# Performance work log

Hardware: AMD Instinct MI355X
Metric: run time of the kernel (lower is better)

## Reference

```python
import jax, jax.numpy as jnp
import numpy as np

B, T, D, F = 4, 2048, 4096, 16384
EQN = 'btd,df->btf'  # fixed einsum equation (contracting axis = D, axis 0 of kernel)


def setup_inputs() -> dict:
    key = jax.random.key(0)
    k1, k2, k3 = jax.random.split(key, 3)
    x = jax.random.normal(k1, (B, T, D), dtype=jnp.float32)
    # int8-quantized kernel weights stored as integers
    kernel = jax.random.randint(k2, (D, F), -127, 128, dtype=jnp.int32).astype(jnp.int8)
    # per-output-channel dequant scale, shape (1, F) per deduce_scale_shape
    scale = jax.random.uniform(k3, (1, F), dtype=jnp.float32, minval=0.5, maxval=1.5)
    return {"x": x, "kernel": kernel, "scale": scale}


def reference(x, kernel, scale):
    # dequantize: cast int kernel to activation dtype, divide by per-channel scale
    k = kernel.astype(x.dtype) / scale  # [D, F]
    return jnp.einsum(EQN, x, k)  # [B, T, F]
```

## Files before the change

kernel.cpp:

```cpp
#include <hip/hip_runtime.h>


namespace {

constexpr int MD = 8192;
constexpr int ND = 16384;
constexpr int KD = 4096;
constexpr int NT = KD / 64;

typedef float fl4 __attribute__((ext_vector_type(4)));
typedef unsigned int u32x4 __attribute__((ext_vector_type(4)));
typedef int i32x4 __attribute__((ext_vector_type(4)));

__device__ __forceinline__ unsigned int pack4(fl4 v, float sc) {
  int q0 = __float2int_rn(v.x * sc);
  int q1 = __float2int_rn(v.y * sc);
  int q2 = __float2int_rn(v.z * sc);
  int q3 = __float2int_rn(v.w * sc);
  return (q0 & 0xFF) | ((q1 & 0xFF) << 8) | ((q2 & 0xFF) << 16) |
         ((q3 & 0xFF) << 24);
}

__global__ __launch_bounds__(256) void quant_x_kernel(
    const float* __restrict__ x, signed char* __restrict__ xq,
    float* __restrict__ xs) {
  const int row = blockIdx.x;
  const int t   = threadIdx.x;
  const float* xr = x + (size_t)row * KD + t * 16;
  fl4 v0 = *(const fl4*)(xr);
  fl4 v1 = *(const fl4*)(xr + 4);
  fl4 v2 = *(const fl4*)(xr + 8);
  fl4 v3 = *(const fl4*)(xr + 12);
  float m = 0.f;
  m = fmaxf(m, fmaxf(fmaxf(fabsf(v0.x), fabsf(v0.y)), fmaxf(fabsf(v0.z), fabsf(v0.w))));
  m = fmaxf(m, fmaxf(fmaxf(fabsf(v1.x), fabsf(v1.y)), fmaxf(fabsf(v1.z), fabsf(v1.w))));
  m = fmaxf(m, fmaxf(fmaxf(fabsf(v2.x), fabsf(v2.y)), fmaxf(fabsf(v2.z), fabsf(v2.w))));
  m = fmaxf(m, fmaxf(fmaxf(fabsf(v3.x), fabsf(v3.y)), fmaxf(fabsf(v3.z), fabsf(v3.w))));
#pragma unroll
  for (int off = 32; off; off >>= 1) m = fmaxf(m, __shfl_xor(m, off));
  __shared__ float red[4];
  if ((t & 63) == 0) red[t >> 6] = m;
  __syncthreads();
  m = fmaxf(fmaxf(red[0], red[1]), fmaxf(red[2], red[3]));
  const float sc = (m > 0.f) ? 127.0f / m : 0.f;
  if (t == 0) xs[row] = (m > 0.f) ? m / 127.0f : 0.f;
  u32x4 o;
  o.x = pack4(v0, sc);
  o.y = pack4(v1, sc);
  o.z = pack4(v2, sc);
  o.w = pack4(v3, sc);
  *(u32x4*)(xq + (size_t)row * KD + t * 16) = o;
}

__global__ __launch_bounds__(256) void transpose_w_kernel(
    const int* __restrict__ W, signed char* __restrict__ WT) {
  constexpr int KC = 64;
  const int nb = blockIdx.x & 63;
  const int kb = blockIdx.x >> 6;
  const int n  = nb * 256 + threadIdx.x;
  const int k0 = kb * KC;
  const int* src = W + (size_t)k0 * ND + n;
  unsigned int buf[16];
#pragma unroll
  for (int i = 0; i < KC; i += 4) {
    unsigned int b0 = (unsigned)src[(size_t)(i + 0) * ND] & 0xFF;
    unsigned int b1 = (unsigned)src[(size_t)(i + 1) * ND] & 0xFF;
    unsigned int b2 = (unsigned)src[(size_t)(i + 2) * ND] & 0xFF;
    unsigned int b3 = (unsigned)src[(size_t)(i + 3) * ND] & 0xFF;
    buf[i >> 2] = b0 | (b1 << 8) | (b2 << 16) | (b3 << 24);
  }
  u32x4* dst = (u32x4*)(WT + (size_t)n * KD + k0);
#pragma unroll
  for (int j = 0; j < 4; ++j) {
    u32x4 o;
    o.x = buf[4 * j + 0];
    o.y = buf[4 * j + 1];
    o.z = buf[4 * j + 2];
    o.w = buf[4 * j + 3];
    dst[j] = o;
  }
}


#define GLL16(g, l)                                                  \
  __builtin_amdgcn_global_load_lds(                                  \
      (const __attribute__((address_space(1))) void*)(g),            \
      (__attribute__((address_space(3))) void*)(l), 16, 0, 0)

#define BARRIER()    __builtin_amdgcn_s_barrier()
#define WAITL(N)     asm volatile("s_waitcnt lgkmcnt(" #N ")")
#define WAITV(N)     asm volatile("s_waitcnt vmcnt(" #N ")")
#define SCHED()      __builtin_amdgcn_sched_barrier(0)
#define PRIO1()      __builtin_amdgcn_s_setprio(1)
#define PRIO0()      __builtin_amdgcn_s_setprio(0)

__device__ __forceinline__ void stage_op(const signed char* g0, char* lbase,
                                         int w) {
  GLL16(g0, lbase + w * 1024);
  GLL16(g0 + (size_t)128 * KD, lbase + 8192 + w * 1024);
}

__global__ __launch_bounds__(512, 2) void gemm_kernel(
    const signed char* __restrict__ Aq8,
    const signed char* __restrict__ Bq8,
    const float* __restrict__ xs,
    const float* __restrict__ scale,
    float* __restrict__ C) {
  __shared__ __align__(16) char Asm[2][16384];
  __shared__ __align__(16) char Bsm[2][16384];

  const int tid  = threadIdx.x;
  const int lane = tid & 63;
  const int w    = tid >> 6;
  const int wm   = w >> 2;
  const int wn   = w & 3;

  const int bid = blockIdx.x;
  const int xcd = bid & 7;
  const int pos = bid >> 3;
  const int tm  = (xcd << 2) | (pos & 3);
  const int tn  = pos >> 2;
  const size_t brow = (size_t)tm * 256;
  const size_t bcol = (size_t)tn * 256;

  const int srow  = w * 16 + (lane >> 2);
  const int sgran = (lane & 3) ^ ((lane >> 3) & 3);
  const signed char* Ag = Aq8 + (brow + srow) * (size_t)KD + sgran * 16;
  const signed char* Bg = Bq8 + (bcol + srow) * (size_t)KD + sgran * 16;

  const int r15  = lane & 15;
  const int kcsw = (((lane >> 4) ^ ((r15 >> 1) & 3)) << 4);

  i32x4 acc[8][4];
#pragma unroll
  for (int i = 0; i < 8; ++i)
#pragma unroll
    for (int j = 0; j < 4; ++j) acc[i][j] = (i32x4){0, 0, 0, 0};

  stage_op(Ag,      &Asm[0][0], w);
  stage_op(Bg,      &Bsm[0][0], w);
  stage_op(Ag + 64, &Asm[1][0], w);
  stage_op(Bg + 64, &Bsm[1][0], w);
  SCHED();
  WAITV(4);
  SCHED();
  BARRIER();
  SCHED();

  i32x4 a[8], b[4];
  {
    const char* A0 = &Asm[0][0] + wm * 8192;
#pragma unroll
    for (int mi = 0; mi < 4; ++mi)
      a[mi] = *(const i32x4*)(A0 + (mi * 16 + r15) * 64 + kcsw);
  }
  SCHED();

#pragma unroll 2
  for (int it = 0; it < NT; ++it) {
    const int h = it & 1;
    const char* Ard  = &Asm[h][0] + wm * 8192;
    const char* ArdN = &Asm[h ^ 1][0] + wm * 8192;
    const char* Brd  = &Bsm[h][0] + wn * 4096;
    const size_t kb2 = (size_t)((it + 2) & (NT - 1)) * 64;

#pragma unroll
    for (int ni = 0; ni < 4; ++ni)
      b[ni] = *(const i32x4*)(Brd + (ni * 16 + r15) * 64 + kcsw);
    SCHED();
#pragma unroll
    for (int mi = 0; mi < 4; ++mi)
      a[4 + mi] = *(const i32x4*)(Ard + ((4 + mi) * 16 + r15) * 64 + kcsw);
    SCHED();
    WAITL(4);
    SCHED();
    PRIO1();
#pragma unroll
    for (int mi = 0; mi < 4; ++mi)
#pragma unroll
      for (int ni = 0; ni < 4; ++ni)
        acc[mi][ni] = __builtin_amdgcn_mfma_i32_16x16x64_i8(
            a[mi], b[ni], acc[mi][ni], 0, 0, 0);
    PRIO0();
    SCHED();
    WAITL(0);
    SCHED();
    PRIO1();
#pragma unroll
    for (int mi = 4; mi < 8; ++mi)
#pragma unroll
      for (int ni = 0; ni < 2; ++ni)
        acc[mi][ni] = __builtin_amdgcn_mfma_i32_16x16x64_i8(
            a[mi], b[ni], acc[mi][ni], 0, 0, 0);
    PRIO0();
    SCHED();
    WAITV(0);
    SCHED();
    BARRIER();
    SCHED();
#pragma unroll
    for (int mi = 0; mi < 4; ++mi)
      a[mi] = *(const i32x4*)(ArdN + (mi * 16 + r15) * 64 + kcsw);
    SCHED();
    BARRIER();
    SCHED();
    stage_op(Ag + kb2, &Asm[h][0], w);
    stage_op(Bg + kb2, &Bsm[h][0], w);
    SCHED();
    PRIO1();
#pragma unroll
    for (int mi = 4; mi < 8; ++mi)
#pragma unroll
      for (int ni = 2; ni < 4; ++ni)
        acc[mi][ni] = __builtin_amdgcn_mfma_i32_16x16x64_i8(
            a[mi], b[ni], acc[mi][ni], 0, 0, 0);
    PRIO0();
    SCHED();
  }

  const int r4 = (lane >> 4) << 2;
  float sxv[8][4];
#pragma unroll
  for (int mi = 0; mi < 8; ++mi)
#pragma unroll
    for (int r = 0; r < 4; ++r)
      sxv[mi][r] = xs[brow + wm * 128 + mi * 16 + r4 + r];
#pragma unroll
  for (int ni = 0; ni < 4; ++ni) {
    const size_t col = bcol + wn * 64 + ni * 16 + r15;
    const float inv = 1.0f / scale[col];
#pragma unroll
    for (int mi = 0; mi < 8; ++mi) {
      float* cp = C + (brow + wm * 128 + mi * 16 + r4) * (size_t)ND + col;
#pragma unroll
      for (int r = 0; r < 4; ++r)
        cp[(size_t)r * ND] = (float)acc[mi][ni][r] * sxv[mi][r] * inv;
    }
  }
}

}

extern "C" void kernel_launch(void* const* d_in, const int* in_sizes, int n_in,
                              void* d_out, int out_size, void* d_ws,
                              size_t ws_size, hipStream_t stream) {
  const float* x     = (const float*)d_in[0];
  const int*   W     = (const int*)d_in[1];
  const float* scale = (const float*)d_in[2];
  float*       out   = (float*)d_out;

  signed char* xq = (signed char*)d_ws;
  signed char* wq = (signed char*)d_ws + (size_t)32 * 1024 * 1024;
  float*       xs = (float*)((char*)d_ws + (size_t)96 * 1024 * 1024);

  quant_x_kernel<<<8192, 256, 0, stream>>>(x, xq, xs);
  transpose_w_kernel<<<4096, 256, 0, stream>>>(W, wq);
  gemm_kernel<<<2048, 512, 0, stream>>>(xq, wq, xs, scale, out);
}
```

Measured before the change: 840.5 us.

## Shrink GEMM block tile to 256x128 with 4 blocks per CU

Changes the int8 GEMM tile from 256x256 to 256x128. Each wave now owns 64x64 instead of 128x64, which halves accumulators and fragment registers and lets launch bounds request 4 blocks per CU with a 4096-block grid. It restructures the LDS staging and the MFMA/ds_read interleave to match. The aim is higher occupancy and better latency hiding, at the cost of lower arithmetic intensity and more global/LDS traffic per MFMA.

```diff
diff --git a/kernel.cpp b/kernel.cpp
--- a/kernel.cpp
+++ b/kernel.cpp
@@ -94,26 +94,20 @@
 #define PRIO1()      __builtin_amdgcn_s_setprio(1)
 #define PRIO0()      __builtin_amdgcn_s_setprio(0)
 
-__device__ __forceinline__ void stage_op(const signed char* g0, char* lbase,
-                                         int w) {
-  GLL16(g0, lbase + w * 1024);
-  GLL16(g0 + (size_t)128 * KD, lbase + 8192 + w * 1024);
-}
-
-__global__ __launch_bounds__(512, 2) void gemm_kernel(
+__global__ __launch_bounds__(512, 4) void gemm_kernel(
     const signed char* __restrict__ Aq8,
     const signed char* __restrict__ Bq8,
     const float* __restrict__ xs,
     const float* __restrict__ scale,
     float* __restrict__ C) {
   __shared__ __align__(16) char Asm[2][16384];
-  __shared__ __align__(16) char Bsm[2][16384];
+  __shared__ __align__(16) char Bsm[2][8192];
 
   const int tid  = threadIdx.x;
   const int lane = tid & 63;
   const int w    = tid >> 6;
-  const int wm   = w >> 2;
-  const int wn   = w & 3;
+  const int wm   = w >> 1;
+  const int wn   = w & 1;
 
   const int bid = blockIdx.x;
   const int xcd = bid & 7;
@@ -121,117 +115,112 @@
   const int tm  = (xcd << 2) | (pos & 3);
   const int tn  = pos >> 2;
   const size_t brow = (size_t)tm * 256;
-  const size_t bcol = (size_t)tn * 256;
-
-  const int srow  = w * 16 + (lane >> 2);
-  const int sgran = (lane & 3) ^ ((lane >> 3) & 3);
+  const size_t bcol = (size_t)tn * 128;
+
+  const int srow  = tid >> 2;
+  const int sgran = (tid & 3) ^ ((tid >> 3) & 3);
   const signed char* Ag = Aq8 + (brow + srow) * (size_t)KD + sgran * 16;
   const signed char* Bg = Bq8 + (bcol + srow) * (size_t)KD + sgran * 16;
 
   const int r15  = lane & 15;
   const int kcsw = (((lane >> 4) ^ ((r15 >> 1) & 3)) << 4);
 
-  i32x4 acc[8][4];
-#pragma unroll
-  for (int i = 0; i < 8; ++i)
+  i32x4 acc[4][4];
+#pragma unroll
+  for (int i = 0; i < 4; ++i)
 #pragma unroll
     for (int j = 0; j < 4; ++j) acc[i][j] = (i32x4){0, 0, 0, 0};
 
-  stage_op(Ag,      &Asm[0][0], w);
-  stage_op(Bg,      &Bsm[0][0], w);
-  stage_op(Ag + 64, &Asm[1][0], w);
-  stage_op(Bg + 64, &Bsm[1][0], w);
-  SCHED();
-  WAITV(4);
+  {
+    GLL16(Ag,                        &Asm[0][0] + w * 1024);
+    GLL16(Ag + (size_t)128 * KD,     &Asm[0][8192] + w * 1024);
+    GLL16(Bg,                        &Bsm[0][0] + w * 1024);
+    GLL16(Ag + 64,                   &Asm[1][0] + w * 1024);
+    GLL16(Ag + (size_t)128 * KD + 64, &Asm[1][8192] + w * 1024);
+    GLL16(Bg + 64,                   &Bsm[1][0] + w * 1024);
+  }
+  SCHED();
+  WAITV(3);
   SCHED();
   BARRIER();
   SCHED();
 
-  i32x4 a[8], b[4];
+  i32x4 a[4], b[4];
   {
-    const char* A0 = &Asm[0][0] + wm * 8192;
-#pragma unroll
-    for (int mi = 0; mi < 4; ++mi)
-      a[mi] = *(const i32x4*)(A0 + (mi * 16 + r15) * 64 + kcsw);
+    const char* Ab = &Asm[0][0] + (wm * 64 + r15) * 64 + kcsw;
+#pragma unroll
+    for (int mi = 0; mi < 4; ++mi) a[mi] = *(const i32x4*)(Ab + mi * 1024);
   }
   SCHED();
 
 #pragma unroll 2
   for (int it = 0; it < NT; ++it) {
     const int h = it & 1;
-    const char* Ard  = &Asm[h][0] + wm * 8192;
-    const char* ArdN = &Asm[h ^ 1][0] + wm * 8192;
-    const char* Brd  = &Bsm[h][0] + wn * 4096;
+    const char* Bb  = &Bsm[h][0] + (wn * 64 + r15) * 64 + kcsw;
+    const char* AbN = &Asm[h ^ 1][0] + (wm * 64 + r15) * 64 + kcsw;
     const size_t kb2 = (size_t)((it + 2) & (NT - 1)) * 64;
 
 #pragma unroll
-    for (int ni = 0; ni < 4; ++ni)
-      b[ni] = *(const i32x4*)(Brd + (ni * 16 + r15) * 64 + kcsw);
-    SCHED();
+    for (int ni = 0; ni < 4; ++ni) b[ni] = *(const i32x4*)(Bb + ni * 1024);
+    SCHED();
+    WAITL(2);
+    SCHED();
+    PRIO1();
 #pragma unroll
     for (int mi = 0; mi < 4; ++mi)
-      a[4 + mi] = *(const i32x4*)(Ard + ((4 + mi) * 16 + r15) * 64 + kcsw);
-    SCHED();
-    WAITL(4);
-    SCHED();
-    PRIO1();
-#pragma unroll
-    for (int mi = 0; mi < 4; ++mi)
-#pragma unroll
-      for (int ni = 0; ni < 4; ++ni)
-        acc[mi][ni] = __builtin_amdgcn_mfma_i32_16x16x64_i8(
-            a[mi], b[ni], acc[mi][ni], 0, 0, 0);
-    PRIO0();
-    SCHED();
-    WAITL(0);
-    SCHED();
-    PRIO1();
-#pragma unroll
-    for (int mi = 4; mi < 8; ++mi)
 #pragma unroll
       for (int ni = 0; ni < 2; ++ni)
         acc[mi][ni] = __builtin_amdgcn_mfma_i32_16x16x64_i8(
             a[mi], b[ni], acc[mi][ni], 0, 0, 0);
     PRIO0();
     SCHED();
-    WAITV(0);
-    SCHED();
-    BARRIER();
-    SCHED();
-#pragma unroll
-    for (int mi = 0; mi < 4; ++mi)
-      a[mi] = *(const i32x4*)(ArdN + (mi * 16 + r15) * 64 + kcsw);
-    SCHED();
-    BARRIER();
-    SCHED();
-    stage_op(Ag + kb2, &Asm[h][0], w);
-    stage_op(Bg + kb2, &Bsm[h][0], w);
+    WAITL(0);
     SCHED();
     PRIO1();
 #pragma unroll
-    for (int mi = 4; mi < 8; ++mi)
+    for (int mi = 0; mi < 2; ++mi)
 #pragma unroll
       for (int ni = 2; ni < 4; ++ni)
         acc[mi][ni] = __builtin_amdgcn_mfma_i32_16x16x64_i8(
             a[mi], b[ni], acc[mi][ni], 0, 0, 0);
     PRIO0();
     SCHED();
+    WAITV(0);
+    SCHED();
+    BARRIER();
+    SCHED();
+    GLL16(Ag + kb2,                        &Asm[h][0] + w * 1024);
+    GLL16(Ag + (size_t)128 * KD + kb2,     &Asm[h][8192] + w * 1024);
+    GLL16(Bg + kb2,                        &Bsm[h][0] + w * 1024);
+    SCHED();
+    PRIO1();
+#pragma unroll
+    for (int mi = 2; mi < 4; ++mi)
+#pragma unroll
+      for (int ni = 2; ni < 4; ++ni)
+        acc[mi][ni] = __builtin_amdgcn_mfma_i32_16x16x64_i8(
+            a[mi], b[ni], acc[mi][ni], 0, 0, 0);
+    PRIO0();
+    SCHED();
+#pragma unroll
+    for (int mi = 0; mi < 4; ++mi) a[mi] = *(const i32x4*)(AbN + mi * 1024);
+    SCHED();
   }
 
   const int r4 = (lane >> 4) << 2;
-  float sxv[8][4];
-#pragma unroll
-  for (int mi = 0; mi < 8; ++mi)
+  float sxv[4][4];
+#pragma unroll
+  for (int mi = 0; mi < 4; ++mi)
 #pragma unroll
     for (int r = 0; r < 4; ++r)
-      sxv[mi][r] = xs[brow + wm * 128 + mi * 16 + r4 + r];
+      sxv[mi][r] = xs[brow + wm * 64 + mi * 16 + r4 + r];
 #pragma unroll
   for (int ni = 0; ni < 4; ++ni) {
     const size_t col = bcol + wn * 64 + ni * 16 + r15;
     const float inv = 1.0f / scale[col];
 #pragma unroll
-    for (int mi = 0; mi < 8; ++mi) {
-      float* cp = C + (brow + wm * 128 + mi * 16 + r4) * (size_t)ND + col;
+    for (int mi = 0; mi < 4; ++mi) {
+      float* cp = C + (brow + wm * 64 + mi * 16 + r4) * (size_t)ND + col;
 #pragma unroll
       for (int r = 0; r < 4; ++r)
         cp[(size_t)r * ND] = (float)acc[mi][ni][r] * sxv[mi][r] * inv;
@@ -255,5 +244,5 @@
 
   quant_x_kernel<<<8192, 256, 0, stream>>>(x, xq, xs);
   transpose_w_kernel<<<4096, 256, 0, stream>>>(W, wq);
-  gemm_kernel<<<2048, 512, 0, stream>>>(xq, wq, xs, scale, out);
-}
+  gemm_kernel<<<4096, 512, 0, stream>>>(xq, wq, xs, scale, out);
+}
```

Result: faster. 745.7 us (-11.3%).
